# Performance work log

Hardware: AMD Instinct MI355X
Metric: run time of the kernel (lower is better)

Reference implementation:

```python
import jax, jax.numpy as jnp
import numpy as np
from jax import lax

B, H, W, C = 16, 32, 32, 256
HEADS = 8
HD = C // HEADS          # attention_head_dim = 32
KSZ = 3                  # conv_kernel_size
DIL = 2                  # dilation_rate
SCALE = HD ** -0.5


def setup_inputs() -> dict:
    key = jax.random.key(0)
    k0, k1, k2, k3 = jax.random.split(key, 4)
    return {
        "query": jax.random.normal(k0, (B, H, W, C), jnp.float32),
        "key_in": jax.random.normal(k1, (B, H, W, C), jnp.float32),
        "value": jax.random.normal(k2, (B, H, W, C), jnp.float32),
        # depthwise conv: kernel [kh, kw, in_ch/groups=1, out_ch=C], plus bias [C]
        "conv_kernel": jax.random.normal(k3, (KSZ, KSZ, 1, C), jnp.float32) * 0.05,
        "conv_bias": jnp.zeros((C,), jnp.float32),
    }


def _dwconv(x, kernel, bias):
    # depthwise dilated conv, padding SAME (Keras Conv2D groups=C)
    y = lax.conv_general_dilated(
        x, kernel,
        window_strides=(1, 1), padding="SAME",
        rhs_dilation=(DIL, DIL),
        dimension_numbers=("NHWC", "HWIO", "NHWC"),
        feature_group_count=C,
    )
    return y + bias


def _to_heads(x):
    # [B,H,W,C] -> [B, heads, S, head_dim]
    return x.reshape(B, H * W, HEADS, HD).transpose(0, 2, 1, 3)


def reference(query, key_in, value, conv_kernel, conv_bias):
    q = _to_heads(query)
    k = _to_heads(_dwconv(key_in, conv_kernel, conv_bias))
    v = _to_heads(_dwconv(value, conv_kernel, conv_bias))
    scores = jnp.einsum("bhqd,bhkd->bhqk", q, k) * SCALE  # [B,heads,S,S]
    attn = jax.nn.softmax(scores, axis=-1)
    out = jnp.einsum("bhqk,bhkd->bhqd", attn, v)          # [B,heads,S,hd]
    return out.transpose(0, 2, 1, 3).reshape(B, H, W, C)
```

## Files before the change

kernel.cpp:

```cpp
#include <hip/hip_runtime.h>

#define B_    16
#define HH    32
#define WW    32
#define CC    256
#define HEADS 8
#define HD    32
#define S_    1024
#define KT    128
#define NITER (S_ / KT)
#define QF    4
#define SCALE_L2E 0.25503486f

typedef unsigned short u16;
typedef unsigned int   u32;
typedef __attribute__((ext_vector_type(8))) short short8;
typedef __attribute__((ext_vector_type(4))) float f32x4;

__device__ __forceinline__ u16 f2bf(float f) {
    u32 x = __float_as_uint(f);
    return (u16)((x + 0x7fffu + ((x >> 16) & 1u)) >> 16);
}
__device__ __forceinline__ u32 pack2bf(float lo, float hi) {
    return (u32)f2bf(lo) | ((u32)f2bf(hi) << 16);
}

__global__ __launch_bounds__(512, 2) void fused_kernel(
    const float* __restrict__ query,
    const float* __restrict__ key_in, const float* __restrict__ value,
    const float* __restrict__ ck, const float* __restrict__ cb,
    float* __restrict__ out)
{
    __shared__ __align__(16) u16 Klds[S_][HD];
    __shared__ __align__(16) u16 Vt[HD][S_ + 8];

    const int tid  = threadIdx.x;
    const int blk  = blockIdx.x;
    const int half = blk & 1;
    const int h    = (blk >> 1) & 7;
    const int b    = blk >> 4;

    {
        const int t  = tid >> 8;
        const int r8 = tid & 255;
        const int x  = (r8 >> 3) & 31;
        const int cq = r8 & 7;
        const float* __restrict__ src = t ? value : key_in;
        const size_t base = ((size_t)b * HH) * WW * CC + (size_t)h * HD + cq * 4;

        float4 w9[9];
        #pragma unroll
        for (int j = 0; j < 9; j++)
            w9[j] = *(const float4*)(ck + j * CC + h * HD + cq * 4);
        const float4 bias = *(const float4*)(cb + h * HD + cq * 4);

        auto tap = [&](int yy, int xx) -> float4 {
            if (yy < 0 || yy >= HH || xx < 0 || xx >= WW)
                return make_float4(0.f, 0.f, 0.f, 0.f);
            return *(const float4*)(src + base + ((size_t)yy * WW + xx) * CC);
        };

        #pragma unroll
        for (int par = 0; par < 2; par++) {
            float4 W[3][3];
            #pragma unroll
            for (int kh = 0; kh < 3; kh++)
                #pragma unroll
                for (int kw = 0; kw < 3; kw++)
                    W[kh][kw] = tap(par - 2 + 2 * kh, x - 2 + 2 * kw);
            #pragma unroll
            for (int y = par; y < HH; y += 2) {
                float4 acc = bias;
                #pragma unroll
                for (int kh = 0; kh < 3; kh++)
                    #pragma unroll
                    for (int kw = 0; kw < 3; kw++) {
                        float4 v = W[kh][kw], w = w9[kh * 3 + kw];
                        acc.x += w.x * v.x; acc.y += w.y * v.y;
                        acc.z += w.z * v.z; acc.w += w.w * v.w;
                    }
                const int pix = y * WW + x;
                if (t == 0) {
                    *(uint2*)&Klds[pix][cq * 4] =
                        make_uint2(pack2bf(acc.x * SCALE_L2E, acc.y * SCALE_L2E),
                                   pack2bf(acc.z * SCALE_L2E, acc.w * SCALE_L2E));
                } else {
                    const int k5  = pix & 31;
                    const int col = (pix & ~31) | ((k5 & 12) << 1)
                                  | ((k5 & 16) >> 2) | (k5 & 3);
                    Vt[cq * 4 + 0][col] = f2bf(acc.x);
                    Vt[cq * 4 + 1][col] = f2bf(acc.y);
                    Vt[cq * 4 + 2][col] = f2bf(acc.z);
                    Vt[cq * 4 + 3][col] = f2bf(acc.w);
                }
                #pragma unroll
                for (int kh = 0; kh < 2; kh++)
                    #pragma unroll
                    for (int kw = 0; kw < 3; kw++)
                        W[kh][kw] = W[kh + 1][kw];
                #pragma unroll
                for (int kw = 0; kw < 3; kw++)
                    W[2][kw] = tap(y + 4, x - 2 + 2 * kw);
            }
        }
    }
    __syncthreads();

    const int lane = tid & 63;
    const int wv   = tid >> 6;
    const int q15  = lane & 15;
    const int quad = lane >> 4;
    const int q0w  = half * 512 + wv * 64;

    short8 qf[QF];
    #pragma unroll
    for (int f = 0; f < QF; f++) {
        const float* qp = query + ((size_t)(b * S_ + q0w + f * 16 + q15)) * CC
                          + h * HD + quad * 8;
        float4 a = *(const float4*)(qp);
        float4 c = *(const float4*)(qp + 4);
        short8 v;
        v[0] = (short)f2bf(a.x); v[1] = (short)f2bf(a.y);
        v[2] = (short)f2bf(a.z); v[3] = (short)f2bf(a.w);
        v[4] = (short)f2bf(c.x); v[5] = (short)f2bf(c.y);
        v[6] = (short)f2bf(c.z); v[7] = (short)f2bf(c.w);
        qf[f] = v;
    }

    short8 ones;
    #pragma unroll
    for (int j = 0; j < 8; j++) ones[j] = (short)0x3F80;

    f32x4 Ot[QF][2];
    f32x4 Dsum[QF];
    #pragma unroll
    for (int f = 0; f < QF; f++) {
        Ot[f][0] = (f32x4)0.f; Ot[f][1] = (f32x4)0.f; Dsum[f] = (f32x4)0.f;
    }

    for (int it = 0; it < NITER; it++) {
        const int kt0 = it * KT;

        short8 kfr0[4], kfr1[4];
        #pragma unroll
        for (int c = 0; c < 4; c++) {
            kfr0[c] = *(const short8*)&Klds[kt0 + c * 32 + q15][quad * 8];
            kfr1[c] = *(const short8*)&Klds[kt0 + c * 32 + 16 + q15][quad * 8];
        }

        #pragma unroll
        for (int c = 0; c < 4; c++) {
            short8 vf0 = *(const short8*)&Vt[q15][kt0 + c * 32 + quad * 8];
            short8 vf1 = *(const short8*)&Vt[16 + q15][kt0 + c * 32 + quad * 8];
            #pragma unroll
            for (int f = 0; f < QF; f++) {
                f32x4 s0 = __builtin_amdgcn_mfma_f32_16x16x32_bf16(kfr0[c], qf[f], (f32x4)0.f, 0, 0, 0);
                f32x4 s1 = __builtin_amdgcn_mfma_f32_16x16x32_bf16(kfr1[c], qf[f], (f32x4)0.f, 0, 0, 0);
                #pragma unroll
                for (int r = 0; r < 4; r++) {
                    s0[r] = __builtin_amdgcn_exp2f(s0[r]);
                    s1[r] = __builtin_amdgcn_exp2f(s1[r]);
                }
                union { u32 u[4]; short8 s8; } pk;
                pk.u[0] = __builtin_amdgcn_perm(__float_as_uint(s0[1]),
                                                __float_as_uint(s0[0]), 0x07060302u);
                pk.u[1] = __builtin_amdgcn_perm(__float_as_uint(s0[3]),
                                                __float_as_uint(s0[2]), 0x07060302u);
                pk.u[2] = __builtin_amdgcn_perm(__float_as_uint(s1[1]),
                                                __float_as_uint(s1[0]), 0x07060302u);
                pk.u[3] = __builtin_amdgcn_perm(__float_as_uint(s1[3]),
                                                __float_as_uint(s1[2]), 0x07060302u);
                Ot[f][0] = __builtin_amdgcn_mfma_f32_16x16x32_bf16(vf0, pk.s8, Ot[f][0], 0, 0, 0);
                Ot[f][1] = __builtin_amdgcn_mfma_f32_16x16x32_bf16(vf1, pk.s8, Ot[f][1], 0, 0, 0);
                Dsum[f]  = __builtin_amdgcn_mfma_f32_16x16x32_bf16(ones, pk.s8, Dsum[f], 0, 0, 0);
            }
        }
    }

    #pragma unroll
    for (int f = 0; f < QF; f++) {
        float inv = 1.0f / Dsum[f][0];
        int qg = q0w + f * 16 + q15;
        float* op = out + ((size_t)(b * S_ + qg)) * CC + h * HD;
        #pragma unroll
        for (int h2 = 0; h2 < 2; h2++)
            #pragma unroll
            for (int r = 0; r < 4; r++)
                op[h2 * 16 + quad * 4 + r] = Ot[f][h2][r] * inv;
    }
}

extern "C" void kernel_launch(void* const* d_in, const int* in_sizes, int n_in,
                              void* d_out, int out_size, void* d_ws, size_t ws_size,
                              hipStream_t stream)
{
    const float* query  = (const float*)d_in[0];
    const float* key_in = (const float*)d_in[1];
    const float* value  = (const float*)d_in[2];
    const float* ck     = (const float*)d_in[3];
    const float* cb     = (const float*)d_in[4];
    float* out = (float*)d_out;
    (void)d_ws; (void)ws_size;

    fused_kernel<<<B_ * HEADS * 2, 512, 0, stream>>>(
        query, key_in, value, ck, cb, out);
}
```

Before: 129.7 us.

## Pad K LDS rows, prefetch Q before conv, interleave conv row parities

Pads the K tile in shared memory to 40 elements per row so the short8 fragment reads hit fewer LDS bank conflicts. Issues the global query loads at kernel start so their latency overlaps the depthwise-convolution phase. Fuses the even and odd row sweeps of the conv into one loop with two sliding windows, putting more independent loads in flight. This raises register pressure (query fragments plus two 3x3 windows held live) and grows LDS usage, which could hurt occupancy at 2 blocks per CU.

Measured after the change: 129.2 us. About the same (-0.4%).

```diff
diff --git a/kernel.cpp b/kernel.cpp
--- a/kernel.cpp
+++ b/kernel.cpp
@@ -10,6 +10,7 @@
 #define KT    128
 #define NITER (S_ / KT)
 #define QF    4
+#define KP    40
 #define SCALE_L2E 0.25503486f
 
 typedef unsigned short u16;
@@ -31,7 +32,7 @@
     const float* __restrict__ ck, const float* __restrict__ cb,
     float* __restrict__ out)
 {
-    __shared__ __align__(16) u16 Klds[S_][HD];
+    __shared__ __align__(16) u16 Klds[S_][KP];
     __shared__ __align__(16) u16 Vt[HD][S_ + 8];
 
     const int tid  = threadIdx.x;
@@ -39,6 +40,21 @@
     const int half = blk & 1;
     const int h    = (blk >> 1) & 7;
     const int b    = blk >> 4;
+
+    const int lane = tid & 63;
+    const int wv   = tid >> 6;
+    const int q15  = lane & 15;
+    const int quad = lane >> 4;
+    const int q0w  = half * 512 + wv * 64;
+
+    float4 qraw[QF][2];
+    #pragma unroll
+    for (int f = 0; f < QF; f++) {
+        const float* qp = query + ((size_t)(b * S_ + q0w + f * 16 + q15)) * CC
+                          + h * HD + quad * 8;
+        qraw[f][0] = *(const float4*)(qp);
+        qraw[f][1] = *(const float4*)(qp + 4);
+    }
 
     {
         const int t  = tid >> 8;
@@ -59,66 +75,70 @@
                 return make_float4(0.f, 0.f, 0.f, 0.f);
             return *(const float4*)(src + base + ((size_t)yy * WW + xx) * CC);
         };
-
-        #pragma unroll
-        for (int par = 0; par < 2; par++) {
-            float4 W[3][3];
+        auto emit = [&](int y, const float4& acc) {
+            const int pix = y * WW + x;
+            if (t == 0) {
+                *(uint2*)&Klds[pix][cq * 4] =
+                    make_uint2(pack2bf(acc.x * SCALE_L2E, acc.y * SCALE_L2E),
+                               pack2bf(acc.z * SCALE_L2E, acc.w * SCALE_L2E));
+            } else {
+                const int k5  = pix & 31;
+                const int col = (pix & ~31) | ((k5 & 12) << 1)
+                              | ((k5 & 16) >> 2) | (k5 & 3);
+                Vt[cq * 4 + 0][col] = f2bf(acc.x);
+                Vt[cq * 4 + 1][col] = f2bf(acc.y);
+                Vt[cq * 4 + 2][col] = f2bf(acc.z);
+                Vt[cq * 4 + 3][col] = f2bf(acc.w);
+            }
+        };
+
+        float4 W0[3][3], W1[3][3];
+        #pragma unroll
+        for (int kh = 0; kh < 3; kh++)
+            #pragma unroll
+            for (int kw = 0; kw < 3; kw++) {
+                W0[kh][kw] = tap(-2 + 2 * kh, x - 2 + 2 * kw);
+                W1[kh][kw] = tap(-1 + 2 * kh, x - 2 + 2 * kw);
+            }
+        #pragma unroll
+        for (int ys = 0; ys < 16; ys++) {
+            const int y0 = 2 * ys, y1 = 2 * ys + 1;
+            float4 acc0 = bias, acc1 = bias;
             #pragma unroll
             for (int kh = 0; kh < 3; kh++)
                 #pragma unroll
-                for (int kw = 0; kw < 3; kw++)
-                    W[kh][kw] = tap(par - 2 + 2 * kh, x - 2 + 2 * kw);
-            #pragma unroll
-            for (int y = par; y < HH; y += 2) {
-                float4 acc = bias;
-                #pragma unroll
-                for (int kh = 0; kh < 3; kh++)
+                for (int kw = 0; kw < 3; kw++) {
+                    const float4 w = w9[kh * 3 + kw];
+                    const float4 v0 = W0[kh][kw], v1 = W1[kh][kw];
+                    acc0.x += w.x * v0.x; acc0.y += w.y * v0.y;
+                    acc0.z += w.z * v0.z; acc0.w += w.w * v0.w;
+                    acc1.x += w.x * v1.x; acc1.y += w.y * v1.y;
+                    acc1.z += w.z * v1.z; acc1.w += w.w * v1.w;
+                }
+            emit(y0, acc0);
+            emit(y1, acc1);
+            if (ys < 15) {
+                #pragma unroll
+                for (int kh = 0; kh < 2; kh++)
                     #pragma unroll
                     for (int kw = 0; kw < 3; kw++) {
-                        float4 v = W[kh][kw], w = w9[kh * 3 + kw];
-                        acc.x += w.x * v.x; acc.y += w.y * v.y;
-                        acc.z += w.z * v.z; acc.w += w.w * v.w;
+                        W0[kh][kw] = W0[kh + 1][kw];
+                        W1[kh][kw] = W1[kh + 1][kw];
                     }
-                const int pix = y * WW + x;
-                if (t == 0) {
-                    *(uint2*)&Klds[pix][cq * 4] =
-                        make_uint2(pack2bf(acc.x * SCALE_L2E, acc.y * SCALE_L2E),
-                                   pack2bf(acc.z * SCALE_L2E, acc.w * SCALE_L2E));
-                } else {
-                    const int k5  = pix & 31;
-                    const int col = (pix & ~31) | ((k5 & 12) << 1)
-                                  | ((k5 & 16) >> 2) | (k5 & 3);
-                    Vt[cq * 4 + 0][col] = f2bf(acc.x);
-                    Vt[cq * 4 + 1][col] = f2bf(acc.y);
-                    Vt[cq * 4 + 2][col] = f2bf(acc.z);
-                    Vt[cq * 4 + 3][col] = f2bf(acc.w);
+                #pragma unroll
+                for (int kw = 0; kw < 3; kw++) {
+                    W0[2][kw] = tap(y0 + 4, x - 2 + 2 * kw);
+                    W1[2][kw] = tap(y1 + 4, x - 2 + 2 * kw);
                 }
-                #pragma unroll
-                for (int kh = 0; kh < 2; kh++)
-                    #pragma unroll
-                    for (int kw = 0; kw < 3; kw++)
-                        W[kh][kw] = W[kh + 1][kw];
-                #pragma unroll
-                for (int kw = 0; kw < 3; kw++)
-                    W[2][kw] = tap(y + 4, x - 2 + 2 * kw);
             }
         }
     }
     __syncthreads();
 
-    const int lane = tid & 63;
-    const int wv   = tid >> 6;
-    const int q15  = lane & 15;
-    const int quad = lane >> 4;
-    const int q0w  = half * 512 + wv * 64;
-
     short8 qf[QF];
     #pragma unroll
     for (int f = 0; f < QF; f++) {
-        const float* qp = query + ((size_t)(b * S_ + q0w + f * 16 + q15)) * CC
-                          + h * HD + quad * 8;
-        float4 a = *(const float4*)(qp);
-        float4 c = *(const float4*)(qp + 4);
+        const float4 a = qraw[f][0], c = qraw[f][1];
         short8 v;
         v[0] = (short)f2bf(a.x); v[1] = (short)f2bf(a.y);
         v[2] = (short)f2bf(a.z); v[3] = (short)f2bf(a.w);
```
